# Performance work log

Hardware: AMD Instinct MI355X
Metric: run time of the kernel (lower is better)

The kernel has to match this reference:

```python
import jax, jax.numpy as jnp
import numpy as np

B, T, I, H, O = 64, 1024, 64, 512, 24


def _gru_cell(x, h, w_ih, w_hh, b_ih, b_hh):
    # PyTorch GRUCell math. w_ih: [3H, in], w_hh: [3H, H]
    gi = x @ w_ih.T + b_ih   # [B, 3H]
    gh = h @ w_hh.T + b_hh   # [B, 3H]
    i_r, i_z, i_n = jnp.split(gi, 3, axis=-1)
    h_r, h_z, h_n = jnp.split(gh, 3, axis=-1)
    r = jax.nn.sigmoid(i_r + h_r)
    z = jax.nn.sigmoid(i_z + h_z)
    n = jnp.tanh(i_n + r * h_n)
    return (1.0 - z) * n + z * h


def setup_inputs() -> dict:
    key = jax.random.key(0)
    ks = jax.random.split(key, 13)
    s1 = 1.0 / np.sqrt(H)
    u = lambda k, shape: jax.random.uniform(k, shape, jnp.float32, -s1, s1)
    return {
        "x": jax.random.normal(ks[0], (B, T, I), jnp.float32),
        "w_ih1": u(ks[1], (3 * H, I)),
        "w_hh1": u(ks[2], (3 * H, H)),
        "b_ih1": u(ks[3], (3 * H,)),
        "b_hh1": u(ks[4], (3 * H,)),
        "w_ih2": u(ks[5], (3 * H, H)),
        "w_hh2": u(ks[6], (3 * H, H)),
        "b_ih2": u(ks[7], (3 * H,)),
        "b_hh2": u(ks[8], (3 * H,)),
        "w_o1": u(ks[9], (O, H)),
        "b_o1": u(ks[10], (O,)),
        "w_o2": u(ks[11], (O, H)),
        "b_o2": u(ks[12], (O,)),
    }


def reference(x, w_ih1, w_hh1, b_ih1, b_hh1, w_ih2, w_hh2, b_ih2, b_hh2,
              w_o1, b_o1, w_o2, b_o2):
    batch = x.shape[0]
    h0 = jnp.zeros((batch, H), x.dtype)

    def step(carry, x_t):
        h1, h2 = carry
        h1 = _gru_cell(x_t, h1, w_ih1, w_hh1, b_ih1, b_hh1)
        h2 = _gru_cell(h1, h2, w_ih2, w_hh2, b_ih2, b_hh2)
        out = jnp.tanh(h1 @ w_o1.T + b_o1) + jnp.tanh(h2 @ w_o2.T + b_o2)
        return (h1, h2), out

    xs = jnp.transpose(x, (1, 0, 2))  # [T, B, I]
    _, outs = jax.lax.scan(step, (h0, h0), xs)  # outs: [T, B, O]
    return jnp.transpose(outs, (1, 0, 2))  # [B, T, O]
```

## Files before the change

kernel.cpp:

```cpp
#include <hip/hip_runtime.h>

typedef unsigned short u16;
typedef unsigned int u32;
typedef unsigned long long u64;
typedef __attribute__((ext_vector_type(8))) short bf16x8;
typedef __attribute__((ext_vector_type(4))) float f32x4;
typedef __attribute__((ext_vector_type(4))) u32 u32x4;

namespace {
constexpr int kT = 1024, kI = 64, kH = 512, kO = 24;
constexpr int kBH = 64 * kH;
constexpr int kNWG = 100;
constexpr unsigned kBarOff = 16u * (unsigned)kBH * 2u;
}

__device__ __forceinline__ u16 f2bf(float f) {
  union { float f; u32 u; } c; c.f = f;
  u32 u = c.u + 0x7FFFu + ((c.u >> 16) & 1u);
  return (u16)(u >> 16);
}
__device__ __forceinline__ float sigf(float x) { return 1.0f / (1.0f + __expf(-x)); }
__device__ __forceinline__ float tanhf_(float x) {
  float e = __expf(2.0f * x); return 1.0f - 2.0f / (e + 1.0f);
}
__device__ __forceinline__ bf16x8 cvt8(const float* p) {
  const float4 f0 = *reinterpret_cast<const float4*>(p);
  const float4 f1 = *reinterpret_cast<const float4*>(p + 4);
  bf16x8 r;
  r[0] = (short)f2bf(f0.x); r[1] = (short)f2bf(f0.y);
  r[2] = (short)f2bf(f0.z); r[3] = (short)f2bf(f0.w);
  r[4] = (short)f2bf(f1.x); r[5] = (short)f2bf(f1.y);
  r[6] = (short)f2bf(f1.z); r[7] = (short)f2bf(f1.w);
  return r;
}
__device__ __forceinline__ f32x4 mfma(bf16x8 a, bf16x8 b, f32x4 c) {
  return __builtin_amdgcn_mfma_f32_16x16x32_bf16(a, b, c, 0, 0, 0);
}
__device__ __forceinline__ int ldflag(const int* s, int i) {
  return __hip_atomic_load(&s[i], __ATOMIC_RELAXED, __HIP_MEMORY_SCOPE_AGENT);
}
__device__ __forceinline__ void stflag(int* s, int i, int v) {
  __hip_atomic_store(&s[i], v, __ATOMIC_RELAXED, __HIP_MEMORY_SCOPE_AGENT);
}
union V16 { u32x4 u; bf16x8 v; };
__device__ __forceinline__ void fetch4(const u16* p, bf16x8* ch) {
  u32x4 a, b, c, d;
  asm volatile(
    "global_load_dwordx4 %0, %4, off sc0 sc1\n\t"
    "global_load_dwordx4 %1, %4, off offset:64 sc0 sc1\n\t"
    "global_load_dwordx4 %2, %4, off offset:128 sc0 sc1\n\t"
    "global_load_dwordx4 %3, %4, off offset:192 sc0 sc1\n\t"
    "s_waitcnt vmcnt(0)"
    : "=&v"(a), "=&v"(b), "=&v"(c), "=&v"(d) : "v"(p) : "memory");
  V16 t;
  t.u = a; ch[0] = t.v;  t.u = b; ch[1] = t.v;
  t.u = c; ch[2] = t.v;  t.u = d; ch[3] = t.v;
}
__device__ __forceinline__ void fetch8(const u16* p, bf16x8* ch) {
  u32x4 a, b, c, d, e, f, g2, h;
  asm volatile(
    "global_load_dwordx4 %0, %8, off sc0 sc1\n\t"
    "global_load_dwordx4 %1, %8, off offset:64 sc0 sc1\n\t"
    "global_load_dwordx4 %2, %8, off offset:128 sc0 sc1\n\t"
    "global_load_dwordx4 %3, %8, off offset:192 sc0 sc1\n\t"
    "global_load_dwordx4 %4, %8, off offset:256 sc0 sc1\n\t"
    "global_load_dwordx4 %5, %8, off offset:320 sc0 sc1\n\t"
    "global_load_dwordx4 %6, %8, off offset:384 sc0 sc1\n\t"
    "global_load_dwordx4 %7, %8, off offset:448 sc0 sc1\n\t"
    "s_waitcnt vmcnt(0)"
    : "=&v"(a), "=&v"(b), "=&v"(c), "=&v"(d),
      "=&v"(e), "=&v"(f), "=&v"(g2), "=&v"(h) : "v"(p) : "memory");
  V16 t;
  t.u = a; ch[0] = t.v;  t.u = b;  ch[1] = t.v;
  t.u = c; ch[2] = t.v;  t.u = d;  ch[3] = t.v;
  t.u = e; ch[4] = t.v;  t.u = f;  ch[5] = t.v;
  t.u = g2; ch[6] = t.v; t.u = h;  ch[7] = t.v;
}
__device__ __forceinline__ u32 pat3(int t3) {
  return ((u32)t3 & 1u) | ((((u32)t3 >> 1) & 1u) << 16);
}
template<int N>
__device__ __forceinline__ bool tagsok(const bf16x8* ch, u32 pat) {
  bool ok = true;
#pragma unroll
  for (int c = 0; c < N; ++c) {
    union { bf16x8 v; u32 u[4]; } t; t.v = ch[c];
    ok = ok && ((t.u[0] & 0x10001u) == pat) && ((t.u[2] & 0x10001u) == pat);
  }
  return ok;
}
template<int N>
__device__ __forceinline__ void dataD(const u16* p, u32 pat, bf16x8* ch) {
  int spins = 0;
  for (;;) {
    u64 g0 = __hip_atomic_load((const u64*)p, __ATOMIC_RELAXED, __HIP_MEMORY_SCOPE_AGENT);
    if (__all(((u32)g0 & 0x10001u) == pat)) break;
    if ((++spins & 3) == 3) __builtin_amdgcn_s_sleep(1);
  }
  spins = 0;
  for (;;) {
    if constexpr (N == 4) fetch4(p, ch); else fetch8(p, ch);
    if (__all(tagsok<N>(ch, pat))) break;
    if ((++spins & 7) == 7) __builtin_amdgcn_s_sleep(1);
  }
  __asm__ volatile("" ::: "memory");
}
__device__ __forceinline__ void st_h(u16* p, const float* h, int t3) {
  u16 a = (u16)((f2bf(h[0]) & ~1u) | ((u32)t3 & 1u));
  u16 b = (u16)((f2bf(h[1]) & ~1u) | (((u32)t3 >> 1) & 1u));
  u64 v = (u64)a | ((u64)b << 16) | ((u64)f2bf(h[2]) << 32) | ((u64)f2bf(h[3]) << 48);
  __hip_atomic_store((u64*)p, v, __ATOMIC_RELAXED, __HIP_MEMORY_SCOPE_AGENT);
}
__device__ __forceinline__ void throttle8(const int* f, int idx, bool act,
                                          int k, int& bound) {
  if (bound >= k - 7) return;
  for (;;) {
    int v = act ? ldflag(f, idx) : 0x7fffffff;
    if (__all(v >= k - 7)) {
      bound = __all(v >= k - 1) ? (k - 1) : (__all(v >= k - 4) ? (k - 4) : (k - 7));
      break;
    }
    __builtin_amdgcn_s_sleep(2);
  }
}

__global__ __launch_bounds__(256, 1) void stackgru(
    const float* __restrict__ x,
    const float* __restrict__ wih1, const float* __restrict__ whh1,
    const float* __restrict__ bih1, const float* __restrict__ bhh1,
    const float* __restrict__ wih2, const float* __restrict__ whh2,
    const float* __restrict__ bih2, const float* __restrict__ bhh2,
    const float* __restrict__ wo1, const float* __restrict__ bo1,
    const float* __restrict__ wo2, const float* __restrict__ bo2,
    float* __restrict__ out, u16* __restrict__ hbuf, int* __restrict__ ctl)
{
  __shared__ float red[4][3][4][64][4];
  __shared__ float redx[2][4][64][4];
  __shared__ float sbias[4][64];
  const int wg = blockIdx.x;
  const int tid = threadIdx.x;
  const int lane = tid & 63;
  const int w = tid >> 6;
  const int l15 = lane & 15;
  const int q = lane >> 4;

  u16* h1b = hbuf;
  u16* h2b = hbuf + 8 * kBH;

  if (wg < 32) {
    const int ub = wg >> 2, g = wg & 3;
    const int U0 = ub * 64;
    const int bb = g * 16 + l15;
    const int kh = w;
    bf16x8 whf[3][4][4];
#pragma unroll
    for (int gg = 0; gg < 3; ++gg)
#pragma unroll
      for (int m = 0; m < 4; ++m)
#pragma unroll
        for (int c = 0; c < 4; ++c)
          whf[gg][m][c] = cvt8(whh1 + (size_t)(gg * kH + U0 + m * 16 + l15) * kH
                               + (kh * 4 + c) * 32 + q * 8);
    const bool hasx = (kh == 1 || kh == 2);
    const int xch = kh - 1;
    bf16x8 aihf[3][4];
    if (hasx)
#pragma unroll
      for (int gg = 0; gg < 3; ++gg)
#pragma unroll
        for (int m = 0; m < 4; ++m)
          aihf[gg][m] = cvt8(wih1 + (size_t)(gg * kH + U0 + m * 16 + l15) * kI
                             + xch * 32 + q * 8);
    if (tid < 64) {
      int u = U0 + tid;
      sbias[0][tid] = bih1[u]          + bhh1[u];
      sbias[1][tid] = bih1[kH + u]     + bhh1[kH + u];
      sbias[2][tid] = bih1[2 * kH + u];
      sbias[3][tid] = bhh1[2 * kH + u];
    }
    float h1l[4];
#pragma unroll
    for (int r = 0; r < 4; ++r) h1l[r] = 0.0f;
    __syncthreads();
    const int thridx = (lane < 16) ? (lane * 4 + g) : (64 + g);
    const bool thract = (lane < 17);
    int bound = 0;
    for (int k = 1; k <= kT; ++k) {
      const int t3 = k % 3, t3p = (k - 1) % 3;
      bf16x8 xf;
      if (hasx)
        xf = cvt8(x + ((size_t)bb * kT + (k - 1)) * kI + xch * 32 + q * 8);
      bf16x8 ch[4];
      dataD<4>(h1b + ((k - 1) & 7) * kBH + (size_t)bb * kH + kh * 128 + q * 8,
               pat3(t3p), ch);
      f32x4 aR[4], aZ[4], aN[4];
#pragma unroll
      for (int m = 0; m < 4; ++m) { aR[m] = {0,0,0,0}; aZ[m] = {0,0,0,0}; aN[m] = {0,0,0,0}; }
#pragma unroll
      for (int m = 0; m < 4; ++m)
#pragma unroll
        for (int c = 0; c < 4; ++c) {
          aR[m] = mfma(whf[0][m][c], ch[c], aR[m]);
          aZ[m] = mfma(whf[1][m][c], ch[c], aZ[m]);
          aN[m] = mfma(whf[2][m][c], ch[c], aN[m]);
        }
      if (hasx) {
        f32x4 xN[4];
#pragma unroll
        for (int m = 0; m < 4; ++m) xN[m] = {0,0,0,0};
#pragma unroll
        for (int m = 0; m < 4; ++m) {
          aR[m] = mfma(aihf[0][m], xf, aR[m]);
          aZ[m] = mfma(aihf[1][m], xf, aZ[m]);
          xN[m] = mfma(aihf[2][m], xf, xN[m]);
        }
#pragma unroll
        for (int m = 0; m < 4; ++m)
#pragma unroll
          for (int r = 0; r < 4; ++r) redx[xch][m][lane][r] = xN[m][r];
      }
#pragma unroll
      for (int m = 0; m < 4; ++m)
#pragma unroll
        for (int r = 0; r < 4; ++r) {
          red[kh][0][m][lane][r] = aR[m][r];
          red[kh][1][m][lane][r] = aZ[m][r];
          red[kh][2][m][lane][r] = aN[m][r];
        }
      if (kh == 0) throttle8(ctl, thridx, thract, k, bound);
      __syncthreads();
      {
        float hnew[4];
#pragma unroll
        for (int r = 0; r < 4; ++r) {
          float sR = red[0][0][w][lane][r] + red[1][0][w][lane][r]
                   + red[2][0][w][lane][r] + red[3][0][w][lane][r];
          float sZ = red[0][1][w][lane][r] + red[1][1][w][lane][r]
                   + red[2][1][w][lane][r] + red[3][1][w][lane][r];
          float sN = red[0][2][w][lane][r] + red[1][2][w][lane][r]
                   + red[2][2][w][lane][r] + red[3][2][w][lane][r];
          float sNi = redx[0][w][lane][r] + redx[1][w][lane][r];
          int uu = w * 16 + q * 4 + r;
          float rr = sigf(sR + sbias[0][uu]);
          float zz = sigf(sZ + sbias[1][uu]);
          float nn = tanhf_(sNi + sbias[2][uu] + rr * (sN + sbias[3][uu]));
          float h  = (1.0f - zz) * nn + zz * h1l[r];
          h1l[r] = h; hnew[r] = h;
        }
        st_h(h1b + (k & 7) * kBH + (size_t)bb * kH + U0 + w * 16 + q * 4, hnew, t3);
      }
      __syncthreads();
    }
  } else if (wg < 96) {
    const int j2 = wg - 32;
    const int ub2 = j2 >> 2, g = j2 & 3;
    const int U0 = ub2 * 32;
    const int bb = g * 16 + l15;
    const int kh = w;
    const float* src = (kh < 2) ? wih2 : whh2;
    const int koff = (kh & 1) * 256;
    bf16x8 whf[3][2][8];
#pragma unroll
    for (int gg = 0; gg < 3; ++gg)
#pragma unroll
      for (int m = 0; m < 2; ++m)
#pragma unroll
        for (int c = 0; c < 8; ++c)
          whf[gg][m][c] = cvt8(src + (size_t)(gg * kH + U0 + m * 16 + l15) * kH
                               + koff + c * 32 + q * 8);
    if (tid < 32) {
      int u = U0 + tid;
      sbias[0][tid] = bih2[u]          + bhh2[u];
      sbias[1][tid] = bih2[kH + u]     + bhh2[kH + u];
      sbias[2][tid] = bih2[2 * kH + u];
      sbias[3][tid] = bhh2[2 * kH + u];
    }
    float h2l[4];
#pragma unroll
    for (int r = 0; r < 4; ++r) h2l[r] = 0.0f;
    __syncthreads();
    int bound = 0;
    for (int k = 1; k <= kT; ++k) {
      const int t3 = k % 3, t3p = (k - 1) % 3;
      const u16* base; u32 pat;
      if (kh < 2) { base = h1b + (k & 7) * kBH;       pat = pat3(t3);  }
      else        { base = h2b + ((k - 1) & 7) * kBH; pat = pat3(t3p); }
      bf16x8 ch[8];
      dataD<8>(base + (size_t)bb * kH + koff + q * 8, pat, ch);
      f32x4 a[3][2];
#pragma unroll
      for (int gg = 0; gg < 3; ++gg)
#pragma unroll
        for (int m = 0; m < 2; ++m) a[gg][m] = {0,0,0,0};
#pragma unroll
      for (int m = 0; m < 2; ++m)
#pragma unroll
        for (int c = 0; c < 8; ++c) {
          a[0][m] = mfma(whf[0][m][c], ch[c], a[0][m]);
          a[1][m] = mfma(whf[1][m][c], ch[c], a[1][m]);
          a[2][m] = mfma(whf[2][m][c], ch[c], a[2][m]);
        }
#pragma unroll
      for (int gg = 0; gg < 3; ++gg)
#pragma unroll
        for (int m = 0; m < 2; ++m)
#pragma unroll
          for (int r = 0; r < 4; ++r) red[kh][gg][m][lane][r] = a[gg][m][r];
      if (kh == 0) throttle8(ctl, 64 + g, lane < 1, k, bound);
      __syncthreads();
      if (tid == 0) stflag(ctl, j2, k);
      if (w < 2) {
        const int m = w;
        float hnew[4];
#pragma unroll
        for (int r = 0; r < 4; ++r) {
          float gi0 = red[0][0][m][lane][r] + red[1][0][m][lane][r];
          float gi1 = red[0][1][m][lane][r] + red[1][1][m][lane][r];
          float gi2 = red[0][2][m][lane][r] + red[1][2][m][lane][r];
          float gh0 = red[2][0][m][lane][r] + red[3][0][m][lane][r];
          float gh1 = red[2][1][m][lane][r] + red[3][1][m][lane][r];
          float gh2 = red[2][2][m][lane][r] + red[3][2][m][lane][r];
          int uu = m * 16 + q * 4 + r;
          float rr = sigf(gi0 + gh0 + sbias[0][uu]);
          float zz = sigf(gi1 + gh1 + sbias[1][uu]);
          float nn = tanhf_(gi2 + sbias[2][uu] + rr * (gh2 + sbias[3][uu]));
          float h  = (1.0f - zz) * nn + zz * h2l[r];
          h2l[r] = h; hnew[r] = h;
        }
        st_h(h2b + (k & 7) * kBH + (size_t)bb * kH + U0 + m * 16 + q * 4, hnew, t3);
      }
      __syncthreads();
    }
  } else {
    const int g3 = wg - 96;
    const int bb = g3 * 16 + l15;
    const int mat = w & 1, khh = w >> 1;
    const float* wsel = mat ? wo2 : wo1;
    bf16x8 zf = {0,0,0,0,0,0,0,0};
    bf16x8 wof[2][8];
#pragma unroll
    for (int t = 0; t < 2; ++t)
#pragma unroll
      for (int c = 0; c < 8; ++c) {
        int row = t * 16 + l15;
        wof[t][c] = (row < kO) ? cvt8(wsel + (size_t)row * kH + khh * 256 + c * 32 + q * 8) : zf;
      }
    float bv1[2][4], bv2[2][4];
#pragma unroll
    for (int t = 0; t < 2; ++t)
#pragma unroll
      for (int r = 0; r < 4; ++r) {
        int o = t * 16 + q * 4 + r;
        bv1[t][r] = (o < kO) ? bo1[o] : 0.0f;
        bv2[t][r] = (o < kO) ? bo2[o] : 0.0f;
      }
    const bool fin = (mat == 0 && khh == 0);
    const u16* slab = mat ? h2b : h1b;
    for (int k = 1; k <= kT; ++k) {
      const u32 pat = pat3(k % 3);
      bf16x8 ch[8];
      dataD<8>(slab + (k & 7) * kBH + (size_t)bb * kH + khh * 256 + q * 8, pat, ch);
      f32x4 a0 = {0,0,0,0}, a1 = {0,0,0,0};
#pragma unroll
      for (int c = 0; c < 8; ++c) {
        a0 = mfma(wof[0][c], ch[c], a0);
        a1 = mfma(wof[1][c], ch[c], a1);
      }
      if (!fin) {
        const int s = mat * 2 + khh - 1;
#pragma unroll
        for (int r = 0; r < 4; ++r) {
          red[s][0][0][lane][r] = a0[r];
          red[s][0][1][lane][r] = a1[r];
        }
      }
      __syncthreads();
      if (tid == 0) stflag(ctl, 64 + g3, k);
      if (fin) {
#pragma unroll
        for (int t = 0; t < 2; ++t) {
          int o0 = t * 16 + q * 4;
          if (o0 < kO) {
            f32x4 av = (t == 0) ? a0 : a1;
            float4 ov;
            ov.x = tanhf_(av[0] + red[0][0][t][lane][0] + bv1[t][0]) +
                   tanhf_(red[1][0][t][lane][0] + red[2][0][t][lane][0] + bv2[t][0]);
            ov.y = tanhf_(av[1] + red[0][0][t][lane][1] + bv1[t][1]) +
                   tanhf_(red[1][0][t][lane][1] + red[2][0][t][lane][1] + bv2[t][1]);
            ov.z = tanhf_(av[2] + red[0][0][t][lane][2] + bv1[t][2]) +
                   tanhf_(red[1][0][t][lane][2] + red[2][0][t][lane][2] + bv2[t][2]);
            ov.w = tanhf_(av[3] + red[0][0][t][lane][3] + bv1[t][3]) +
                   tanhf_(red[1][0][t][lane][3] + red[2][0][t][lane][3] + bv2[t][3]);
            *reinterpret_cast<float4*>(out + ((size_t)bb * kT + (k - 1)) * kO + o0) = ov;
          }
        }
      }
      __syncthreads();
    }
  }
}

extern "C" void kernel_launch(void* const* d_in, const int* in_sizes, int n_in,
                              void* d_out, int out_size, void* d_ws, size_t ws_size,
                              hipStream_t stream) {
  (void)in_sizes; (void)n_in; (void)out_size; (void)ws_size;
  hipMemsetAsync(d_ws, 0, kBarOff + 1024, stream);
  hipMemsetAsync((char*)d_ws + 3u * kBH * 2u, 0x01, kBH * 2u, stream);
  hipMemsetAsync((char*)d_ws + 6u * kBH * 2u, 0x01, kBH * 2u, stream);
  hipMemsetAsync((char*)d_ws + (8u + 3u) * kBH * 2u, 0x01, kBH * 2u, stream);
  hipMemsetAsync((char*)d_ws + (8u + 6u) * kBH * 2u, 0x01, kBH * 2u, stream);
  const float* x    = (const float*)d_in[0];
  const float* wih1 = (const float*)d_in[1];
  const float* whh1 = (const float*)d_in[2];
  const float* bih1 = (const float*)d_in[3];
  const float* bhh1 = (const float*)d_in[4];
  const float* wih2 = (const float*)d_in[5];
  const float* whh2 = (const float*)d_in[6];
  const float* bih2 = (const float*)d_in[7];
  const float* bhh2 = (const float*)d_in[8];
  const float* wo1  = (const float*)d_in[9];
  const float* bo1  = (const float*)d_in[10];
  const float* wo2  = (const float*)d_in[11];
  const float* bo2  = (const float*)d_in[12];
  float* out  = (float*)d_out;
  u16* hbuf   = (u16*)d_ws;
  int* ctl    = (int*)((char*)d_ws + kBarOff);
  stackgru<<<dim3(kNWG), dim3(256), 0, stream>>>(
      x, wih1, whh1, bih1, bhh1, wih2, whh2, bih2, bhh2,
      wo1, bo1, wo2, bo2, out, hbuf, ctl);
}
```

Baseline: 3.563 ms.

## Give each layer-1 wave full K to drop LDS reduction and block barriers

Layer-1 work is repartitioned so each wavefront owns a 16-unit by 16-batch tile over the whole hidden dimension. It fetches all 16 chunks of h1 itself and applies the input weights directly. This removes the cross-wave LDS reduction and both __syncthreads per timestep, and every wave now calls throttle on its own. In exchange each wave holds 48 weight fragments in registers and issues larger per-step loads, with a separate poll on a scattered sentinel before fetching. The extra register pressure and more polling traffic per wave may cost latency.

```diff
diff --git a/kernel.cpp b/kernel.cpp
--- a/kernel.cpp
+++ b/kernel.cpp
@@ -76,6 +76,37 @@
   t.u = e; ch[4] = t.v;  t.u = f;  ch[5] = t.v;
   t.u = g2; ch[6] = t.v; t.u = h;  ch[7] = t.v;
 }
+__device__ __forceinline__ void fetch16(const u16* p, bf16x8* ch) {
+  u32x4 t0,t1,t2,t3,t4,t5,t6,t7,t8,t9,t10,t11,t12,t13,t14,t15;
+  asm volatile(
+    "global_load_dwordx4 %0, %16, off sc0 sc1\n\t"
+    "global_load_dwordx4 %1, %16, off offset:64 sc0 sc1\n\t"
+    "global_load_dwordx4 %2, %16, off offset:128 sc0 sc1\n\t"
+    "global_load_dwordx4 %3, %16, off offset:192 sc0 sc1\n\t"
+    "global_load_dwordx4 %4, %16, off offset:256 sc0 sc1\n\t"
+    "global_load_dwordx4 %5, %16, off offset:320 sc0 sc1\n\t"
+    "global_load_dwordx4 %6, %16, off offset:384 sc0 sc1\n\t"
+    "global_load_dwordx4 %7, %16, off offset:448 sc0 sc1\n\t"
+    "global_load_dwordx4 %8, %16, off offset:512 sc0 sc1\n\t"
+    "global_load_dwordx4 %9, %16, off offset:576 sc0 sc1\n\t"
+    "global_load_dwordx4 %10, %16, off offset:640 sc0 sc1\n\t"
+    "global_load_dwordx4 %11, %16, off offset:704 sc0 sc1\n\t"
+    "global_load_dwordx4 %12, %16, off offset:768 sc0 sc1\n\t"
+    "global_load_dwordx4 %13, %16, off offset:832 sc0 sc1\n\t"
+    "global_load_dwordx4 %14, %16, off offset:896 sc0 sc1\n\t"
+    "global_load_dwordx4 %15, %16, off offset:960 sc0 sc1\n\t"
+    "s_waitcnt vmcnt(0)"
+    : "=&v"(t0), "=&v"(t1), "=&v"(t2), "=&v"(t3),
+      "=&v"(t4), "=&v"(t5), "=&v"(t6), "=&v"(t7),
+      "=&v"(t8), "=&v"(t9), "=&v"(t10), "=&v"(t11),
+      "=&v"(t12), "=&v"(t13), "=&v"(t14), "=&v"(t15)
+    : "v"(p) : "memory");
+  V16 u;
+  u.u=t0; ch[0]=u.v;   u.u=t1; ch[1]=u.v;   u.u=t2; ch[2]=u.v;   u.u=t3; ch[3]=u.v;
+  u.u=t4; ch[4]=u.v;   u.u=t5; ch[5]=u.v;   u.u=t6; ch[6]=u.v;   u.u=t7; ch[7]=u.v;
+  u.u=t8; ch[8]=u.v;   u.u=t9; ch[9]=u.v;   u.u=t10; ch[10]=u.v; u.u=t11; ch[11]=u.v;
+  u.u=t12; ch[12]=u.v; u.u=t13; ch[13]=u.v; u.u=t14; ch[14]=u.v; u.u=t15; ch[15]=u.v;
+}
 __device__ __forceinline__ u32 pat3(int t3) {
   return ((u32)t3 & 1u) | ((((u32)t3 >> 1) & 1u) << 16);
 }
@@ -88,6 +119,23 @@
     ok = ok && ((t.u[0] & 0x10001u) == pat) && ((t.u[2] & 0x10001u) == pat);
   }
   return ok;
+}
+__device__ __forceinline__ void pollh(const u16* ps, u32 pat) {
+  int sp = 0;
+  for (;;) {
+    u64 g = __hip_atomic_load((const u64*)ps, __ATOMIC_RELAXED, __HIP_MEMORY_SCOPE_AGENT);
+    if (__all(((u32)g & 0x10001u) == pat)) break;
+    if ((++sp & 7) == 7) __builtin_amdgcn_s_sleep(1);
+  }
+}
+__device__ __forceinline__ void fetchv16(const u16* p, u32 pat, bf16x8* ch) {
+  int sp = 0;
+  for (;;) {
+    fetch16(p, ch);
+    if (__all(tagsok<16>(ch, pat))) break;
+    if ((++sp & 7) == 7) __builtin_amdgcn_s_sleep(1);
+  }
+  __asm__ volatile("" ::: "memory");
 }
 template<int N>
 __device__ __forceinline__ void dataD(const u16* p, u32 pat, bf16x8* ch) {
@@ -135,7 +183,6 @@
     float* __restrict__ out, u16* __restrict__ hbuf, int* __restrict__ ctl)
 {
   __shared__ float red[4][3][4][64][4];
-  __shared__ float redx[2][4][64][4];
   __shared__ float sbias[4][64];
   const int wg = blockIdx.x;
   const int tid = threadIdx.x;
@@ -148,108 +195,66 @@
   u16* h2b = hbuf + 8 * kBH;
 
   if (wg < 32) {
-    const int ub = wg >> 2, g = wg & 3;
-    const int U0 = ub * 64;
+    const int idx = wg * 4 + w;
+    const int ut = idx & 31, U0 = ut * 16;
+    const int g = idx >> 5;
     const int bb = g * 16 + l15;
-    const int kh = w;
-    bf16x8 whf[3][4][4];
+    bf16x8 whf[3][16];
 #pragma unroll
     for (int gg = 0; gg < 3; ++gg)
 #pragma unroll
-      for (int m = 0; m < 4; ++m)
-#pragma unroll
-        for (int c = 0; c < 4; ++c)
-          whf[gg][m][c] = cvt8(whh1 + (size_t)(gg * kH + U0 + m * 16 + l15) * kH
-                               + (kh * 4 + c) * 32 + q * 8);
-    const bool hasx = (kh == 1 || kh == 2);
-    const int xch = kh - 1;
-    bf16x8 aihf[3][4];
-    if (hasx)
-#pragma unroll
-      for (int gg = 0; gg < 3; ++gg)
-#pragma unroll
-        for (int m = 0; m < 4; ++m)
-          aihf[gg][m] = cvt8(wih1 + (size_t)(gg * kH + U0 + m * 16 + l15) * kI
-                             + xch * 32 + q * 8);
-    if (tid < 64) {
-      int u = U0 + tid;
-      sbias[0][tid] = bih1[u]          + bhh1[u];
-      sbias[1][tid] = bih1[kH + u]     + bhh1[kH + u];
-      sbias[2][tid] = bih1[2 * kH + u];
-      sbias[3][tid] = bhh1[2 * kH + u];
-    }
-    float h1l[4];
-#pragma unroll
-    for (int r = 0; r < 4; ++r) h1l[r] = 0.0f;
-    __syncthreads();
+      for (int c = 0; c < 16; ++c)
+        whf[gg][c] = cvt8(whh1 + (size_t)(gg * kH + U0 + l15) * kH + c * 32 + q * 8);
+    bf16x8 aihf[3][2];
+#pragma unroll
+    for (int gg = 0; gg < 3; ++gg)
+#pragma unroll
+      for (int c = 0; c < 2; ++c)
+        aihf[gg][c] = cvt8(wih1 + (size_t)(gg * kH + U0 + l15) * kI + c * 32 + q * 8);
+    float br[4], bz[4], bni[4], bnh[4], h1l[4];
+#pragma unroll
+    for (int r = 0; r < 4; ++r) {
+      int u = U0 + q * 4 + r;
+      br[r]  = bih1[u]          + bhh1[u];
+      bz[r]  = bih1[kH + u]     + bhh1[kH + u];
+      bni[r] = bih1[2 * kH + u];
+      bnh[r] = bhh1[2 * kH + u];
+      h1l[r] = 0.0f;
+    }
+    const int sU = (lane & 31) * 16;
+    const int sB = (lane >> 5) * 15;
     const int thridx = (lane < 16) ? (lane * 4 + g) : (64 + g);
     const bool thract = (lane < 17);
     int bound = 0;
     for (int k = 1; k <= kT; ++k) {
       const int t3 = k % 3, t3p = (k - 1) % 3;
-      bf16x8 xf;
-      if (hasx)
-        xf = cvt8(x + ((size_t)bb * kT + (k - 1)) * kI + xch * 32 + q * 8);
-      bf16x8 ch[4];
-      dataD<4>(h1b + ((k - 1) & 7) * kBH + (size_t)bb * kH + kh * 128 + q * 8,
-               pat3(t3p), ch);
-      f32x4 aR[4], aZ[4], aN[4];
-#pragma unroll
-      for (int m = 0; m < 4; ++m) { aR[m] = {0,0,0,0}; aZ[m] = {0,0,0,0}; aN[m] = {0,0,0,0}; }
-#pragma unroll
-      for (int m = 0; m < 4; ++m)
-#pragma unroll
-        for (int c = 0; c < 4; ++c) {
-          aR[m] = mfma(whf[0][m][c], ch[c], aR[m]);
-          aZ[m] = mfma(whf[1][m][c], ch[c], aZ[m]);
-          aN[m] = mfma(whf[2][m][c], ch[c], aN[m]);
-        }
-      if (hasx) {
-        f32x4 xN[4];
-#pragma unroll
-        for (int m = 0; m < 4; ++m) xN[m] = {0,0,0,0};
-#pragma unroll
-        for (int m = 0; m < 4; ++m) {
-          aR[m] = mfma(aihf[0][m], xf, aR[m]);
-          aZ[m] = mfma(aihf[1][m], xf, aZ[m]);
-          xN[m] = mfma(aihf[2][m], xf, xN[m]);
-        }
-#pragma unroll
-        for (int m = 0; m < 4; ++m)
-#pragma unroll
-          for (int r = 0; r < 4; ++r) redx[xch][m][lane][r] = xN[m][r];
-      }
-#pragma unroll
-      for (int m = 0; m < 4; ++m)
-#pragma unroll
-        for (int r = 0; r < 4; ++r) {
-          red[kh][0][m][lane][r] = aR[m][r];
-          red[kh][1][m][lane][r] = aZ[m][r];
-          red[kh][2][m][lane][r] = aN[m][r];
-        }
-      if (kh == 0) throttle8(ctl, thridx, thract, k, bound);
-      __syncthreads();
-      {
-        float hnew[4];
-#pragma unroll
-        for (int r = 0; r < 4; ++r) {
-          float sR = red[0][0][w][lane][r] + red[1][0][w][lane][r]
-                   + red[2][0][w][lane][r] + red[3][0][w][lane][r];
-          float sZ = red[0][1][w][lane][r] + red[1][1][w][lane][r]
-                   + red[2][1][w][lane][r] + red[3][1][w][lane][r];
-          float sN = red[0][2][w][lane][r] + red[1][2][w][lane][r]
-                   + red[2][2][w][lane][r] + red[3][2][w][lane][r];
-          float sNi = redx[0][w][lane][r] + redx[1][w][lane][r];
-          int uu = w * 16 + q * 4 + r;
-          float rr = sigf(sR + sbias[0][uu]);
-          float zz = sigf(sZ + sbias[1][uu]);
-          float nn = tanhf_(sNi + sbias[2][uu] + rr * (sN + sbias[3][uu]));
-          float h  = (1.0f - zz) * nn + zz * h1l[r];
-          h1l[r] = h; hnew[r] = h;
-        }
-        st_h(h1b + (k & 7) * kBH + (size_t)bb * kH + U0 + w * 16 + q * 4, hnew, t3);
-      }
-      __syncthreads();
+      const float* xs = x + ((size_t)bb * kT + (k - 1)) * kI + q * 8;
+      bf16x8 xf0 = cvt8(xs), xf1 = cvt8(xs + 32);
+      const u16* pb = h1b + ((k - 1) & 7) * kBH;
+      pollh(pb + (size_t)(g * 16 + sB) * kH + sU, pat3(t3p));
+      bf16x8 ch[16];
+      fetchv16(pb + (size_t)bb * kH + q * 8, pat3(t3p), ch);
+      f32x4 aR = {0,0,0,0}, aZ = {0,0,0,0}, aNh = {0,0,0,0}, aNi = {0,0,0,0};
+#pragma unroll
+      for (int c = 0; c < 16; ++c) {
+        aR  = mfma(whf[0][c], ch[c], aR);
+        aZ  = mfma(whf[1][c], ch[c], aZ);
+        aNh = mfma(whf[2][c], ch[c], aNh);
+      }
+      aR  = mfma(aihf[0][0], xf0, aR);  aR  = mfma(aihf[0][1], xf1, aR);
+      aZ  = mfma(aihf[1][0], xf0, aZ);  aZ  = mfma(aihf[1][1], xf1, aZ);
+      aNi = mfma(aihf[2][0], xf0, aNi); aNi = mfma(aihf[2][1], xf1, aNi);
+      throttle8(ctl, thridx, thract, k, bound);
+      float hnew[4];
+#pragma unroll
+      for (int r = 0; r < 4; ++r) {
+        float rr = sigf(aR[r] + br[r]);
+        float zz = sigf(aZ[r] + bz[r]);
+        float nn = tanhf_(aNi[r] + bni[r] + rr * (aNh[r] + bnh[r]));
+        float h  = (1.0f - zz) * nn + zz * h1l[r];
+        h1l[r] = h; hnew[r] = h;
+      }
+      st_h(h1b + (k & 7) * kBH + (size_t)bb * kH + U0 + q * 4, hnew, t3);
     }
   } else if (wg < 96) {
     const int j2 = wg - 32;
```

Result: slower. 5.798 ms (+62.7%).
